# Optimization experiments

Measured on AMD Instinct MI355X. Metric: run time of the kernel, lower is better.

## Reference

```python
import jax, jax.numpy as jnp
import numpy as np

B, L, H = 4, 1024, 1024          # docs, seq_len, hidden (LUKE-large)
NH, M, E, R = 16, 64, 24, 512    # attn heads, mentions/doc, entities/doc, pairs/doc
EMB, BLK, NCLS = 768, 64, 97     # embed_size, block_size, num_class


def setup_inputs() -> dict:
    key = jax.random.key(0)
    ks = jax.random.split(key, 10)
    s = 0.02
    return {
        "seq_lhs": jax.random.normal(ks[0], (B, L, H), jnp.float32),
        "ent_lhs": jax.random.normal(ks[1], (B, M, H), jnp.float32),
        "ent_to_seq_attn": jax.random.uniform(ks[2], (B, NH, M, L), jnp.float32),
        "entity_id_labels": jax.random.randint(ks[3], (B, M), 0, E),
        "hts": jax.random.randint(ks[4], (B, R, 2), 0, E),
        "Wh": jax.random.normal(ks[5], (2 * H, EMB), jnp.float32) * s,
        "bh": jnp.zeros((EMB,), jnp.float32),
        "Wt": jax.random.normal(ks[6], (2 * H, EMB), jnp.float32) * s,
        "bt": jnp.zeros((EMB,), jnp.float32),
        "Wb": jax.random.normal(ks[7], (EMB * BLK, 768), jnp.float32) * s,
        "bb": jnp.zeros((768,), jnp.float32),
        "Wc": jax.random.normal(ks[8], (768, NCLS), jnp.float32) * s,
        "bc": jnp.zeros((NCLS,), jnp.float32),
    }


def reference(seq_lhs, ent_lhs, ent_to_seq_attn, entity_id_labels, hts,
              Wh, bh, Wt, bt, Wb, bb, Wc, bc):
    dt = seq_lhs.dtype
    # mention -> entity segment mask [B, E, M]
    mask = entity_id_labels[:, None, :] == jnp.arange(E)[None, :, None]
    counts = mask.sum(-1)  # [B, E]
    # entity embedding: logsumexp over its mentions (== identity for 1 mention),
    # zeros for entities with no mentions
    masked = jnp.where(mask[..., None], ent_lhs[:, None, :, :], jnp.asarray(-1e30, dt))
    ent_emb = jax.scipy.special.logsumexp(masked, axis=2)           # [B, E, H]
    ent_emb = jnp.where((counts > 0)[..., None], ent_emb, jnp.asarray(0.0, dt))
    # entity -> seq attention: mean over mentions, zeros for empty entities
    mf = mask.astype(dt)
    ent_attn = jnp.einsum('bem,bhml->behl', mf, ent_to_seq_attn)    # [B, E, NH, L]
    ent_attn = ent_attn / jnp.maximum(counts, 1)[:, :, None, None].astype(dt)
    # gather per-pair head/tail embeddings and attentions
    h_idx, t_idx = hts[..., 0], hts[..., 1]                          # [B, R]
    hs = jnp.take_along_axis(ent_emb, h_idx[..., None], axis=1)      # [B, R, H]
    ts = jnp.take_along_axis(ent_emb, t_idx[..., None], axis=1)
    ha = jnp.take_along_axis(ent_attn, h_idx[..., None, None], axis=1)  # [B, R, NH, L]
    ta = jnp.take_along_axis(ent_attn, t_idx[..., None, None], axis=1)
    ht = (ha * ta).mean(2)                                           # [B, R, L]
    ht = ht / (ht.sum(-1, keepdims=True) + 1e-5)
    rel = jnp.einsum('bld,brl->brd', seq_lhs, ht)                    # [B, R, H]
    # head/tail extractors with context concat
    he = jnp.tanh(jnp.concatenate([hs, rel], -1) @ Wh + bh)          # [B, R, EMB]
    te = jnp.tanh(jnp.concatenate([ts, rel], -1) @ Wt + bt)
    K = EMB // BLK
    b1 = he.reshape(B * R, K, BLK)
    b2 = te.reshape(B * R, K, BLK)
    bl = (b1[:, :, :, None] * b2[:, :, None, :]).reshape(B * R, EMB * BLK)
    embeds = bl @ Wb + bb                                            # [B*R, 768]
    return embeds @ Wc + bc                                          # [B*R, NCLS]
```

## Files before the change

kernel.cpp:

```cpp
#include <hip/hip_runtime.h>
#include <stdint.h>
#include <math.h>

#define B_    4
#define L_    1024
#define H_    1024
#define NH_   16
#define M_    64
#define E_    24
#define R_    512
#define EMB_  768
#define BLK_  64
#define NCLS_ 97
#define NR_   2048
#define KBIG_ 49152
#define NCH_  768

typedef unsigned short ushort_t;
typedef short bf16x8 __attribute__((ext_vector_type(8)));
typedef float f32x4  __attribute__((ext_vector_type(4)));

__device__ __forceinline__ float bf2f(ushort_t u) {
    return __uint_as_float(((unsigned)u) << 16);
}
__device__ __forceinline__ ushort_t f2bf_rne(float f) {
    unsigned u = __float_as_uint(f);
    return (ushort_t)((u + 0x7fffu + ((u >> 16) & 1u)) >> 16);
}
__device__ __forceinline__ ushort_t f2bf_fast(float f) {
    unsigned u = __float_as_uint(f);
    return (ushort_t)((u + 0x8000u) >> 16);
}

__global__ __launch_bounds__(256) void k_transpose_cvt(
    const float* __restrict__ in, ushort_t* __restrict__ out, int rows, int cols)
{
    __shared__ float tile[32][33];
    int batch = blockIdx.z;
    in  += (size_t)batch * rows * cols;
    out += (size_t)batch * rows * cols;
    int c0 = blockIdx.x * 32, r0 = blockIdx.y * 32;
    int tx = threadIdx.x & 31, ty = threadIdx.x >> 5;
#pragma unroll
    for (int dy = 0; dy < 32; dy += 8)
        tile[ty + dy][tx] = in[(size_t)(r0 + ty + dy) * cols + (c0 + tx)];
    __syncthreads();
#pragma unroll
    for (int dy = 0; dy < 32; dy += 8)
        out[(size_t)(c0 + ty + dy) * rows + (r0 + tx)] = f2bf_rne(tile[tx][ty + dy]);
}

__global__ __launch_bounds__(256) void k_ent_emb(
    const float* __restrict__ ent_lhs, const int* __restrict__ labels,
    float* __restrict__ ent_emb)
{
    int b = blockIdx.x / E_, e = blockIdx.x % E_;
    __shared__ int list[M_];
    __shared__ int cnt;
    if (threadIdx.x == 0) cnt = 0;
    __syncthreads();
    if (threadIdx.x < M_ && labels[b * M_ + threadIdx.x] == e) {
        int p = atomicAdd(&cnt, 1);
        list[p] = threadIdx.x;
    }
    __syncthreads();
    int n = cnt;
    const float* base = ent_lhs + (size_t)b * M_ * H_;
    float* outp = ent_emb + ((size_t)b * E_ + e) * H_;
    for (int h = threadIdx.x; h < H_; h += blockDim.x) {
        if (n == 0) { outp[h] = 0.f; continue; }
        float mx = -1e30f;
        for (int i = 0; i < n; i++) mx = fmaxf(mx, base[(size_t)list[i] * H_ + h]);
        float s = 0.f;
        for (int i = 0; i < n; i++) s += __expf(base[(size_t)list[i] * H_ + h] - mx);
        outp[h] = mx + __logf(s);
    }
}

__global__ __launch_bounds__(256) void k_ent_attn(
    const float* __restrict__ attn, const int* __restrict__ labels,
    float* __restrict__ ent_attn)
{
    int idx = blockIdx.x;
    int nh = idx % NH_;
    int be = idx / NH_;
    int e = be % E_, b = be / E_;
    __shared__ int list[M_];
    __shared__ int cnt;
    if (threadIdx.x == 0) cnt = 0;
    __syncthreads();
    if (threadIdx.x < M_ && labels[b * M_ + threadIdx.x] == e) {
        int p = atomicAdd(&cnt, 1);
        list[p] = threadIdx.x;
    }
    __syncthreads();
    int n = cnt;
    float inv = 1.f / fmaxf((float)n, 1.f);
    const float* base = attn + ((size_t)b * NH_ + nh) * M_ * L_;
    float* outp = ent_attn + (((size_t)b * E_ + e) * NH_ + nh) * L_;
    for (int l = threadIdx.x; l < L_; l += blockDim.x) {
        float s = 0.f;
        for (int i = 0; i < n; i++) s += base[(size_t)list[i] * L_ + l];
        outp[l] = s * inv;
    }
}

__global__ __launch_bounds__(256) void k_ht(
    const float* __restrict__ ent_attn, const int* __restrict__ hts,
    ushort_t* __restrict__ ht_bf)
{
    int b = blockIdx.x / R_, r = blockIdx.x % R_;
    int h = hts[((size_t)b * R_ + r) * 2 + 0];
    int t = hts[((size_t)b * R_ + r) * 2 + 1];
    const float* ha = ent_attn + ((size_t)b * E_ + h) * NH_ * L_;
    const float* ta = ent_attn + ((size_t)b * E_ + t) * NH_ * L_;
    float vals[4];
    float local = 0.f;
#pragma unroll
    for (int p = 0; p < 4; p++) {
        int l = threadIdx.x + p * 256;
        float s = 0.f;
#pragma unroll
        for (int nh = 0; nh < NH_; nh++) s += ha[nh * L_ + l] * ta[nh * L_ + l];
        s *= (1.f / NH_);
        vals[p] = s;
        local += s;
    }
    __shared__ float red[4];
    float s = local;
#pragma unroll
    for (int off = 32; off > 0; off >>= 1) s += __shfl_down(s, off, 64);
    if ((threadIdx.x & 63) == 0) red[threadIdx.x >> 6] = s;
    __syncthreads();
    float tot = red[0] + red[1] + red[2] + red[3];
    float inv = 1.f / (tot + 1e-5f);
    ushort_t* outp = ht_bf + ((size_t)b * R_ + r) * L_;
#pragma unroll
    for (int p = 0; p < 4; p++) {
        int l = threadIdx.x + p * 256;
        outp[l] = f2bf_rne(vals[p] * inv);
    }
}

__global__ __launch_bounds__(256) void k_gather(
    const float* __restrict__ ent_emb, const int* __restrict__ hts,
    ushort_t* __restrict__ A1, ushort_t* __restrict__ A2)
{
    int n = blockIdx.x;
    int b = n / R_, r = n % R_;
    int h = hts[((size_t)b * R_ + r) * 2 + 0];
    int t = hts[((size_t)b * R_ + r) * 2 + 1];
    const float* eh = ent_emb + ((size_t)b * E_ + h) * H_;
    const float* et = ent_emb + ((size_t)b * E_ + t) * H_;
    for (int i = threadIdx.x; i < H_; i += 256) {
        A1[(size_t)n * 2048 + i] = f2bf_rne(eh[i]);
        A2[(size_t)n * 2048 + i] = f2bf_rne(et[i]);
    }
}

template <bool BIAS, bool TANH, bool DUAL>
__global__ __launch_bounds__(256) void k_gemm(
    const ushort_t* __restrict__ A, long sA, int lda,
    const ushort_t* __restrict__ Bt, long sB, int ldb,
    int K,
    const float* __restrict__ bias0, const float* __restrict__ bias1,
    ushort_t* __restrict__ C0, ushort_t* __restrict__ C1, long sC, int ldc)
{
    __shared__ ushort_t As[128 * 72];
    __shared__ ushort_t Bs[128 * 72];
    const int tid = threadIdx.x;
    const int lane = tid & 63, wid = tid >> 6;
    const int wr = wid >> 1, wc = wid & 1;
    const int z = blockIdx.z;
    const int m0 = blockIdx.y * 128, n0 = blockIdx.x * 128;
    A  += (long)z * sA;
    Bt += (long)z * sB;

    const f32x4 zero = {0.f, 0.f, 0.f, 0.f};
    f32x4 acc[4][4];
#pragma unroll
    for (int i = 0; i < 4; i++)
#pragma unroll
        for (int j = 0; j < 4; j++) acc[i][j] = zero;

    const int mrow = wr * 64 + (lane & 15);
    const int nrow = wc * 64 + (lane & 15);
    const int koff = (lane >> 4) * 8;

    for (int k0 = 0; k0 < K; k0 += 64) {
        __syncthreads();
#pragma unroll
        for (int p = 0; p < 4; p++) {
            int idx = tid + p * 256;
            int row = idx >> 3, seg = idx & 7;
            *reinterpret_cast<int4*>(&As[row * 72 + seg * 8]) =
                *reinterpret_cast<const int4*>(&A[(long)(m0 + row) * lda + k0 + seg * 8]);
            *reinterpret_cast<int4*>(&Bs[row * 72 + seg * 8]) =
                *reinterpret_cast<const int4*>(&Bt[(long)(n0 + row) * ldb + k0 + seg * 8]);
        }
        __syncthreads();
#pragma unroll
        for (int ks = 0; ks < 2; ks++) {
            bf16x8 af[4], bfg[4];
#pragma unroll
            for (int mt = 0; mt < 4; mt++)
                af[mt] = *reinterpret_cast<const bf16x8*>(&As[(mrow + mt * 16) * 72 + ks * 32 + koff]);
#pragma unroll
            for (int nt = 0; nt < 4; nt++)
                bfg[nt] = *reinterpret_cast<const bf16x8*>(&Bs[(nrow + nt * 16) * 72 + ks * 32 + koff]);
#pragma unroll
            for (int mt = 0; mt < 4; mt++)
#pragma unroll
                for (int nt = 0; nt < 4; nt++)
                    acc[mt][nt] = __builtin_amdgcn_mfma_f32_16x16x32_bf16(
                        af[mt], bfg[nt], acc[mt][nt], 0, 0, 0);
        }
    }

    const float* bias = BIAS ? (z ? bias1 : bias0) : nullptr;
#pragma unroll
    for (int mt = 0; mt < 4; mt++) {
#pragma unroll
        for (int nt = 0; nt < 4; nt++) {
#pragma unroll
            for (int rg = 0; rg < 4; rg++) {
                int row = m0 + wr * 64 + mt * 16 + (lane >> 4) * 4 + rg;
                int col = n0 + wc * 64 + nt * 16 + (lane & 15);
                float v = acc[mt][nt][rg];
                if (BIAS) v += bias[col];
                if (TANH) {
                    float vc = fminf(fmaxf(v, -15.f), 15.f);
                    float ex = __expf(2.f * vc);
                    v = (ex - 1.f) / (ex + 1.f);
                }
                ushort_t bv = f2bf_rne(v);
                C0[(long)z * sC + (long)row * ldc + col] = bv;
                if (DUAL) C1[(long)z * sC + (long)row * ldc + col] = bv;
            }
        }
    }
}

__global__ __launch_bounds__(256) void k_bilinear(
    const ushort_t* __restrict__ he, const ushort_t* __restrict__ te,
    const ushort_t* __restrict__ Wbt, float* __restrict__ embeds)
{
    __shared__ ushort_t TEs[128 * 72];
    __shared__ ushort_t HEs[128 * 72];
    const int tid = threadIdx.x;
    const int lane = tid & 63, wid = tid >> 6;
    const int wr = wid >> 1, wc = wid & 1;
    const int d0 = blockIdx.x * 128, n0 = blockIdx.y * 128;
    const int c0 = blockIdx.z * 96, cend = c0 + 96;

    const f32x4 zero = {0.f, 0.f, 0.f, 0.f};
    f32x4 acc[4][4];
#pragma unroll
    for (int i = 0; i < 4; i++)
#pragma unroll
        for (int j = 0; j < 4; j++) acc[i][j] = zero;

    const int mrow = wr * 64 + (lane & 15);
    const int drow = d0 + wc * 64 + (lane & 15);
    const int koff = (lane >> 4) * 8;

    int c = c0;
    while (c < cend) {
        const int k  = c >> 6;
        const int i0 = c & 63;
        const int i1 = min(64, i0 + (cend - c));
        __syncthreads();
#pragma unroll
        for (int p = 0; p < 4; p++) {
            int idx = tid + p * 256;
            int row = idx >> 3, seg = idx & 7;
            *reinterpret_cast<int4*>(&TEs[row * 72 + seg * 8]) =
                *reinterpret_cast<const int4*>(&te[(long)(n0 + row) * EMB_ + k * 64 + seg * 8]);
            *reinterpret_cast<int4*>(&HEs[row * 72 + seg * 8]) =
                *reinterpret_cast<const int4*>(&he[(long)(n0 + row) * EMB_ + k * 64 + seg * 8]);
        }
        __syncthreads();

        bf16x8 tef[4][2];
#pragma unroll
        for (int mt = 0; mt < 4; mt++)
#pragma unroll
            for (int ks = 0; ks < 2; ks++)
                tef[mt][ks] = *reinterpret_cast<const bf16x8*>(
                    &TEs[(mrow + mt * 16) * 72 + ks * 32 + koff]);

        for (int i = i0; i < i1; i++) {
            const long kkbase = (long)(k * 64 + i) * 64;
            bf16x8 bfr[4][2];
#pragma unroll
            for (int nt = 0; nt < 4; nt++)
#pragma unroll
                for (int ks = 0; ks < 2; ks++)
                    bfr[nt][ks] = *reinterpret_cast<const bf16x8*>(
                        &Wbt[(long)(drow + nt * 16) * KBIG_ + kkbase + ks * 32 + koff]);
            float hef[4];
#pragma unroll
            for (int mt = 0; mt < 4; mt++)
                hef[mt] = bf2f(HEs[(mrow + mt * 16) * 72 + i]);
#pragma unroll
            for (int mt = 0; mt < 4; mt++) {
#pragma unroll
                for (int ks = 0; ks < 2; ks++) {
                    bf16x8 a;
#pragma unroll
                    for (int q = 0; q < 8; q++)
                        a[q] = (short)f2bf_fast(bf2f((ushort_t)tef[mt][ks][q]) * hef[mt]);
#pragma unroll
                    for (int nt = 0; nt < 4; nt++)
                        acc[mt][nt] = __builtin_amdgcn_mfma_f32_16x16x32_bf16(
                            a, bfr[nt][ks], acc[mt][nt], 0, 0, 0);
                }
            }
        }
        c += (i1 - i0);
    }

#pragma unroll
    for (int mt = 0; mt < 4; mt++)
#pragma unroll
        for (int nt = 0; nt < 4; nt++)
#pragma unroll
            for (int rg = 0; rg < 4; rg++) {
                int n = n0 + wr * 64 + mt * 16 + (lane >> 4) * 4 + rg;
                int d = d0 + wc * 64 + nt * 16 + (lane & 15);
                atomicAdd(&embeds[(long)n * EMB_ + d], acc[mt][nt][rg]);
            }
}

__global__ __launch_bounds__(128) void k_final(
    const float* __restrict__ embeds, const float* __restrict__ bb,
    const float* __restrict__ Wc, const float* __restrict__ bc,
    float* __restrict__ out)
{
    int n = blockIdx.x;
    __shared__ float row[EMB_];
    for (int i = threadIdx.x; i < EMB_; i += 128)
        row[i] = embeds[(size_t)n * EMB_ + i] + bb[i];
    __syncthreads();
    int j = threadIdx.x;
    if (j < NCLS_) {
        float s = bc[j];
#pragma unroll 8
        for (int d = 0; d < EMB_; d++) s += row[d] * Wc[d * NCLS_ + j];
        out[(size_t)n * NCLS_ + j] = s;
    }
}

extern "C" void kernel_launch(void* const* d_in, const int* in_sizes, int n_in,
                              void* d_out, int out_size, void* d_ws, size_t ws_size,
                              hipStream_t stream)
{
    (void)in_sizes; (void)n_in; (void)out_size; (void)ws_size;
    const float* seq    = (const float*)d_in[0];
    const float* entl   = (const float*)d_in[1];
    const float* attn   = (const float*)d_in[2];
    const int*   labels = (const int*)d_in[3];
    const int*   hts    = (const int*)d_in[4];
    const float* Wh     = (const float*)d_in[5];
    const float* bh     = (const float*)d_in[6];
    const float* Wt     = (const float*)d_in[7];
    const float* bt     = (const float*)d_in[8];
    const float* Wb     = (const float*)d_in[9];
    const float* bb     = (const float*)d_in[10];
    const float* Wc     = (const float*)d_in[11];
    const float* bc     = (const float*)d_in[12];
    float* out = (float*)d_out;

    char* ws = (char*)d_ws;
    size_t off = 0;
    auto alloc = [&](size_t bytes) -> char* {
        char* p = ws + off;
        off += (bytes + 255) & ~(size_t)255;
        return p;
    };
    float*    ent_emb  = (float*)alloc((size_t)B_ * E_ * H_ * 4);
    float*    ent_attn = (float*)alloc((size_t)B_ * E_ * NH_ * L_ * 4);
    ushort_t* ht_bf    = (ushort_t*)alloc((size_t)B_ * R_ * L_ * 2);
    ushort_t* seq_t    = (ushort_t*)alloc((size_t)B_ * H_ * L_ * 2);
    ushort_t* A1       = (ushort_t*)alloc((size_t)NR_ * 2048 * 2);
    ushort_t* A2       = (ushort_t*)alloc((size_t)NR_ * 2048 * 2);
    ushort_t* Whb      = (ushort_t*)alloc((size_t)EMB_ * 2048 * 2);
    ushort_t* Wtb      = (ushort_t*)alloc((size_t)EMB_ * 2048 * 2);
    ushort_t* he_bf    = (ushort_t*)alloc((size_t)NR_ * EMB_ * 2);
    ushort_t* te_bf    = (ushort_t*)alloc((size_t)NR_ * EMB_ * 2);
    ushort_t* Wbt      = (ushort_t*)alloc((size_t)EMB_ * KBIG_ * 2);
    float*    embeds   = (float*)alloc((size_t)NR_ * EMB_ * 4);

    k_transpose_cvt<<<dim3(H_ / 32, L_ / 32, B_), 256, 0, stream>>>(seq, seq_t, L_, H_);
    k_transpose_cvt<<<dim3(EMB_ / 32, 2048 / 32, 1), 256, 0, stream>>>(Wh, Whb, 2048, EMB_);
    k_transpose_cvt<<<dim3(EMB_ / 32, 2048 / 32, 1), 256, 0, stream>>>(Wt, Wtb, 2048, EMB_);
    k_transpose_cvt<<<dim3(EMB_ / 32, KBIG_ / 32, 1), 256, 0, stream>>>(Wb, Wbt, KBIG_, EMB_);

    k_ent_emb<<<B_ * E_, 256, 0, stream>>>(entl, labels, ent_emb);
    k_ent_attn<<<B_ * E_ * NH_, 256, 0, stream>>>(attn, labels, ent_attn);

    k_ht<<<NR_, 256, 0, stream>>>(ent_attn, hts, ht_bf);
    k_gather<<<NR_, 256, 0, stream>>>(ent_emb, hts, A1, A2);

    k_gemm<false, false, true><<<dim3(H_ / 128, R_ / 128, B_), 256, 0, stream>>>(
        ht_bf, (long)R_ * L_, L_,
        seq_t, (long)H_ * L_, L_,
        L_, nullptr, nullptr,
        A1 + 1024, A2 + 1024, (long)R_ * 2048, 2048);

    k_gemm<true, true, false><<<dim3(EMB_ / 128, NR_ / 128, 2), 256, 0, stream>>>(
        A1, (long)NR_ * 2048, 2048,
        Whb, (long)EMB_ * 2048, 2048,
        2048, bh, bt,
        he_bf, nullptr, (long)NR_ * EMB_, EMB_);

    (void)hipMemsetAsync(embeds, 0, (size_t)NR_ * EMB_ * 4, stream);
    k_bilinear<<<dim3(EMB_ / 128, NR_ / 128, 8), 256, 0, stream>>>(he_bf, te_bf, Wbt, embeds);

    k_final<<<NR_, 128, 0, stream>>>(embeds, bb, Wc, bc, out);
}
```

Before: 738.8 us.

## Widen transpose tiles, pack bf16 scaling, split-K partial buffers, regroup bilinear blocks

The transpose kernel now uses 64x64 tiles and writes 16 bf16 values per thread as vector stores. The bilinear A-fragment scaling packs two bf16 values at a time with a perm instruction, which removes per-element conversions. When the workspace is large enough, each split-K slice writes its own partial buffer instead of using float atomics, k_final sums the slices, and the memset is skipped. The bilinear grid is flattened so the 8 K-splits of one output tile are adjacent, which should help L2 reuse of he/te. The cost is 8x more partial-buffer traffic and a small rounding change (truncation instead of round-half-up).

Result: no change. 727.4 us (-1.6%).

```diff
diff --git a/kernel.cpp b/kernel.cpp
--- a/kernel.cpp
+++ b/kernel.cpp
@@ -17,6 +17,7 @@
 #define NCH_  768
 
 typedef unsigned short ushort_t;
+typedef unsigned int uint_t;
 typedef short bf16x8 __attribute__((ext_vector_type(8)));
 typedef float f32x4  __attribute__((ext_vector_type(4)));
 
@@ -27,27 +28,33 @@
     unsigned u = __float_as_uint(f);
     return (ushort_t)((u + 0x7fffu + ((u >> 16) & 1u)) >> 16);
 }
-__device__ __forceinline__ ushort_t f2bf_fast(float f) {
-    unsigned u = __float_as_uint(f);
-    return (ushort_t)((u + 0x8000u) >> 16);
+__device__ __forceinline__ uint_t pack2_scale(uint_t tw, float h) {
+    float lo = __uint_as_float(tw << 16) * h;
+    float hi = __uint_as_float(tw & 0xffff0000u) * h;
+    return __builtin_amdgcn_perm(__float_as_uint(hi), __float_as_uint(lo), 0x07060302u);
 }
 
 __global__ __launch_bounds__(256) void k_transpose_cvt(
     const float* __restrict__ in, ushort_t* __restrict__ out, int rows, int cols)
 {
-    __shared__ float tile[32][33];
+    __shared__ float t[64][65];
     int batch = blockIdx.z;
     in  += (size_t)batch * rows * cols;
     out += (size_t)batch * rows * cols;
-    int c0 = blockIdx.x * 32, r0 = blockIdx.y * 32;
-    int tx = threadIdx.x & 31, ty = threadIdx.x >> 5;
-#pragma unroll
-    for (int dy = 0; dy < 32; dy += 8)
-        tile[ty + dy][tx] = in[(size_t)(r0 + ty + dy) * cols + (c0 + tx)];
-    __syncthreads();
-#pragma unroll
-    for (int dy = 0; dy < 32; dy += 8)
-        out[(size_t)(c0 + ty + dy) * rows + (r0 + tx)] = f2bf_rne(tile[tx][ty + dy]);
+    int c0 = blockIdx.x * 64, r0 = blockIdx.y * 64;
+    int tx = threadIdx.x & 63, ty = threadIdx.x >> 6;
+#pragma unroll
+    for (int dr = 0; dr < 64; dr += 4)
+        t[dr + ty][tx] = in[(size_t)(r0 + dr + ty) * cols + (c0 + tx)];
+    __syncthreads();
+    int c = threadIdx.x >> 2;
+    int rk = (threadIdx.x & 3) * 16;
+    ushort_t us[16];
+#pragma unroll
+    for (int q = 0; q < 16; q++) us[q] = f2bf_rne(t[rk + q][c]);
+    ushort_t* op = &out[(size_t)(c0 + c) * rows + r0 + rk];
+    *reinterpret_cast<int4*>(op)     = *reinterpret_cast<const int4*>(&us[0]);
+    *reinterpret_cast<int4*>(op + 8) = *reinterpret_cast<const int4*>(&us[8]);
 }
 
 __global__ __launch_bounds__(256) void k_ent_emb(
@@ -243,15 +250,18 @@
 
 __global__ __launch_bounds__(256) void k_bilinear(
     const ushort_t* __restrict__ he, const ushort_t* __restrict__ te,
-    const ushort_t* __restrict__ Wbt, float* __restrict__ embeds)
+    const ushort_t* __restrict__ Wbt, float* __restrict__ embeds8, int splitz)
 {
     __shared__ ushort_t TEs[128 * 72];
     __shared__ ushort_t HEs[128 * 72];
     const int tid = threadIdx.x;
     const int lane = tid & 63, wid = tid >> 6;
     const int wr = wid >> 1, wc = wid & 1;
-    const int d0 = blockIdx.x * 128, n0 = blockIdx.y * 128;
-    const int c0 = blockIdx.z * 96, cend = c0 + 96;
+    const int bid = blockIdx.x;
+    const int z = bid & 7;
+    const int w = bid >> 3;
+    const int d0 = (w % 6) * 128, n0 = (w / 6) * 128;
+    const int c0 = z * 96, cend = c0 + 96;
 
     const f32x4 zero = {0.f, 0.f, 0.f, 0.f};
     f32x4 acc[4][4];
@@ -281,12 +291,12 @@
         }
         __syncthreads();
 
-        bf16x8 tef[4][2];
+        uint4 tef[4][2];
 #pragma unroll
         for (int mt = 0; mt < 4; mt++)
 #pragma unroll
             for (int ks = 0; ks < 2; ks++)
-                tef[mt][ks] = *reinterpret_cast<const bf16x8*>(
+                tef[mt][ks] = *reinterpret_cast<const uint4*>(
                     &TEs[(mrow + mt * 16) * 72 + ks * 32 + koff]);
 
         for (int i = i0; i < i1; i++) {
@@ -306,20 +316,23 @@
             for (int mt = 0; mt < 4; mt++) {
 #pragma unroll
                 for (int ks = 0; ks < 2; ks++) {
-                    bf16x8 a;
-#pragma unroll
-                    for (int q = 0; q < 8; q++)
-                        a[q] = (short)f2bf_fast(bf2f((ushort_t)tef[mt][ks][q]) * hef[mt]);
+                    uint4 t = tef[mt][ks];
+                    union { uint_t u[4]; bf16x8 v; } a;
+                    a.u[0] = pack2_scale(t.x, hef[mt]);
+                    a.u[1] = pack2_scale(t.y, hef[mt]);
+                    a.u[2] = pack2_scale(t.z, hef[mt]);
+                    a.u[3] = pack2_scale(t.w, hef[mt]);
 #pragma unroll
                     for (int nt = 0; nt < 4; nt++)
                         acc[mt][nt] = __builtin_amdgcn_mfma_f32_16x16x32_bf16(
-                            a, bfr[nt][ks], acc[mt][nt], 0, 0, 0);
+                            a.v, bfr[nt][ks], acc[mt][nt], 0, 0, 0);
                 }
             }
         }
         c += (i1 - i0);
     }
 
+    float* outp = embeds8 + (splitz ? (long)z * NR_ * EMB_ : 0l);
 #pragma unroll
     for (int mt = 0; mt < 4; mt++)
 #pragma unroll
@@ -328,19 +341,24 @@
             for (int rg = 0; rg < 4; rg++) {
                 int n = n0 + wr * 64 + mt * 16 + (lane >> 4) * 4 + rg;
                 int d = d0 + wc * 64 + nt * 16 + (lane & 15);
-                atomicAdd(&embeds[(long)n * EMB_ + d], acc[mt][nt][rg]);
+                if (splitz) outp[(long)n * EMB_ + d] = acc[mt][nt][rg];
+                else        atomicAdd(&outp[(long)n * EMB_ + d], acc[mt][nt][rg]);
             }
 }
 
 __global__ __launch_bounds__(128) void k_final(
-    const float* __restrict__ embeds, const float* __restrict__ bb,
+    const float* __restrict__ embeds8, int nz, const float* __restrict__ bb,
     const float* __restrict__ Wc, const float* __restrict__ bc,
     float* __restrict__ out)
 {
     int n = blockIdx.x;
     __shared__ float row[EMB_];
-    for (int i = threadIdx.x; i < EMB_; i += 128)
-        row[i] = embeds[(size_t)n * EMB_ + i] + bb[i];
+    for (int i = threadIdx.x; i < EMB_; i += 128) {
+        float s = bb[i];
+        for (int zz = 0; zz < nz; zz++)
+            s += embeds8[(size_t)zz * NR_ * EMB_ + (size_t)n * EMB_ + i];
+        row[i] = s;
+    }
     __syncthreads();
     int j = threadIdx.x;
     if (j < NCLS_) {
@@ -355,7 +373,7 @@
                               void* d_out, int out_size, void* d_ws, size_t ws_size,
                               hipStream_t stream)
 {
-    (void)in_sizes; (void)n_in; (void)out_size; (void)ws_size;
+    (void)in_sizes; (void)n_in; (void)out_size;
     const float* seq    = (const float*)d_in[0];
     const float* entl   = (const float*)d_in[1];
     const float* attn   = (const float*)d_in[2];
@@ -389,12 +407,14 @@
     ushort_t* he_bf    = (ushort_t*)alloc((size_t)NR_ * EMB_ * 2);
     ushort_t* te_bf    = (ushort_t*)alloc((size_t)NR_ * EMB_ * 2);
     ushort_t* Wbt      = (ushort_t*)alloc((size_t)EMB_ * KBIG_ * 2);
-    float*    embeds   = (float*)alloc((size_t)NR_ * EMB_ * 4);
-
-    k_transpose_cvt<<<dim3(H_ / 32, L_ / 32, B_), 256, 0, stream>>>(seq, seq_t, L_, H_);
-    k_transpose_cvt<<<dim3(EMB_ / 32, 2048 / 32, 1), 256, 0, stream>>>(Wh, Whb, 2048, EMB_);
-    k_transpose_cvt<<<dim3(EMB_ / 32, 2048 / 32, 1), 256, 0, stream>>>(Wt, Wtb, 2048, EMB_);
-    k_transpose_cvt<<<dim3(EMB_ / 32, KBIG_ / 32, 1), 256, 0, stream>>>(Wb, Wbt, KBIG_, EMB_);
+    size_t embeds_off = off;
+    int splitz = (ws_size >= embeds_off + (size_t)8 * NR_ * EMB_ * 4) ? 1 : 0;
+    float* embeds8 = (float*)alloc((size_t)(splitz ? 8 : 1) * NR_ * EMB_ * 4);
+
+    k_transpose_cvt<<<dim3(H_ / 64, L_ / 64, B_), 256, 0, stream>>>(seq, seq_t, L_, H_);
+    k_transpose_cvt<<<dim3(EMB_ / 64, 2048 / 64, 1), 256, 0, stream>>>(Wh, Whb, 2048, EMB_);
+    k_transpose_cvt<<<dim3(EMB_ / 64, 2048 / 64, 1), 256, 0, stream>>>(Wt, Wtb, 2048, EMB_);
+    k_transpose_cvt<<<dim3(EMB_ / 64, KBIG_ / 64, 1), 256, 0, stream>>>(Wb, Wbt, KBIG_, EMB_);
 
     k_ent_emb<<<B_ * E_, 256, 0, stream>>>(entl, labels, ent_emb);
     k_ent_attn<<<B_ * E_ * NH_, 256, 0, stream>>>(attn, labels, ent_attn);
@@ -414,8 +434,9 @@
         2048, bh, bt,
         he_bf, nullptr, (long)NR_ * EMB_, EMB_);
 
-    (void)hipMemsetAsync(embeds, 0, (size_t)NR_ * EMB_ * 4, stream);
-    k_bilinear<<<dim3(EMB_ / 128, NR_ / 128, 8), 256, 0, stream>>>(he_bf, te_bf, Wbt, embeds);
-
-    k_final<<<NR_, 128, 0, stream>>>(embeds, bb, Wc, bc, out);
-}
+    if (!splitz)
+        (void)hipMemsetAsync(embeds8, 0, (size_t)NR_ * EMB_ * 4, stream);
+    k_bilinear<<<768, 256, 0, stream>>>(he_bf, te_bf, Wbt, embeds8, splitz);
+
+    k_final<<<NR_, 128, 0, stream>>>(embeds8, splitz ? 8 : 1, bb, Wc, bc, out);
+}
```
